# Optimization experiments

Measured on AMD Instinct MI355X. Metric: run time of the kernel, lower is better.

The kernel has to match this reference:

```python
import jax, jax.numpy as jnp
import numpy as np

WINDOW_SIZE, SM, PS = 8, 2, 2  # window_size, spatial_merge_size, patch_size
SMU = SM * SM  # spatial_merge_unit


def _window_index(grid_thw):
    """Numpy port of get_window_index; returns permutation of arange(S)."""
    vmws = WINDOW_SIZE // SM // PS  # 2
    out, wid = [], 0
    for t, h, w in grid_thw:
        lh, lw = h // SM, w // SM
        idx = np.arange(t * lh * lw).reshape(t, lh, lw)
        ph = vmws - lh % vmws
        pw = vmws - lw % vmws
        nh, nw = (lh + ph) // vmws, (lw + pw) // vmws
        pad = np.full((t, lh + ph, lw + pw), -100, dtype=np.int64)
        pad[:, :lh, :lw] = idx
        pad = pad.reshape(t, nh, vmws, nw, vmws).transpose(0, 1, 3, 2, 4).reshape(-1)
        out.append(pad[pad != -100] + wid)
        wid += t * lh * lw
    return np.concatenate(out).astype(np.int32)


def setup_inputs() -> dict:
    key = jax.random.key(0)
    ks = jax.random.split(key, 5)
    B, T, C, H = 1, 16384, 1280, 16
    D = C // H  # 80
    grid_thw = np.array([[1, 256, 256]], dtype=np.int64)  # llm grid 128x128 -> S=16384
    wi = _window_index(grid_thw)
    x = jax.random.normal(ks[0], (B, T, C), jnp.float32)
    cos = jax.random.normal(ks[1], (B * T, 1, D), jnp.float32)
    sin = jax.random.normal(ks[2], (B * T, 1, D), jnp.float32)
    W_qkv = jax.random.normal(ks[3], (C, 3 * C), jnp.float32) * (C ** -0.5)
    W_proj = jax.random.normal(ks[4], (C, C), jnp.float32) * (C ** -0.5)
    # each window: (vmws*vmws) merged tokens * SMU patches = 16 tokens
    block_size = (WINDOW_SIZE // SM // PS) ** 2 * SMU
    return {"x": x, "cos": cos, "sin": sin, "W_qkv": W_qkv, "W_proj": W_proj,
            "window_index": jnp.asarray(wi), "block_size": block_size}


def reference(x, cos, sin, W_qkv, W_proj, window_index, block_size):
    B, T, C = x.shape
    S = B * T
    D = cos.shape[-1]
    H = C // D
    # window reorder (gather)
    xr = x.reshape(S, C)[window_index]
    qkv = (xr @ W_qkv).reshape(S, 3, H, D)
    q, k, v = qkv[:, 0], qkv[:, 1], qkv[:, 2]
    # module's (unusual) q/k mixing 'rotary'
    cw, sw = cos[window_index], sin[window_index]  # (S,1,D) broadcast over heads
    qr = q * cw + k * sw
    kr = k * cw - q * sw
    # block-diagonal attention: uniform 16-token windows -> reshape, no SxS mask
    nb = S // block_size
    qb = qr.reshape(nb, block_size, H, D)
    kb = kr.reshape(nb, block_size, H, D)
    vb = v.reshape(nb, block_size, H, D)
    att = jnp.einsum('bqhd,bkhd->bhqk', qb, kb) * (D ** -0.5)
    att = jax.nn.softmax(att, axis=-1)
    y = jnp.einsum('bhqk,bkhd->bqhd', att, vb).reshape(S, C)
    # undo window reorder
    y = y[jnp.argsort(window_index)]
    return y.reshape(B, T, C) @ W_proj
```

## Files before the change

kernel.cpp:

```cpp
#include <hip/hip_runtime.h>
#include <hip/hip_bf16.h>

#define S_TOK   16384
#define C_DIM   1280
#define C3_DIM  3840
#define H_DIM   16
#define D_DIM   80
#define BLK     16

using u16x8  = __attribute__((ext_vector_type(8))) unsigned short;
using bf16x8 = __attribute__((ext_vector_type(8))) __bf16;
using f32x4  = __attribute__((ext_vector_type(4))) float;

__device__ __forceinline__ unsigned short f2bf(float f) {
    return __bfloat16_as_ushort(__float2bfloat16(f));
}
__device__ __forceinline__ float bf2f(unsigned short u) {
    unsigned int x = (unsigned int)u << 16;
    return __builtin_bit_cast(float, x);
}
__device__ __forceinline__ void gload_lds16(const unsigned short* g, unsigned short* l) {
    __builtin_amdgcn_global_load_lds(
        (const __attribute__((address_space(1))) void*)g,
        (__attribute__((address_space(3))) void*)l, 16, 0, 0);
}

__global__ __launch_bounds__(256) void transpose_cvt(
    const float* __restrict__ W, unsigned short* __restrict__ WT, int K, int N)
{
    __shared__ float tile[32][33];
    const int n0 = blockIdx.x * 32, k0 = blockIdx.y * 32;
    const int tx = threadIdx.x & 31, ty = threadIdx.x >> 5;
#pragma unroll
    for (int i = ty; i < 32; i += 8)
        tile[i][tx] = W[(size_t)(k0 + i) * N + n0 + tx];
    __syncthreads();
#pragma unroll
    for (int i = ty; i < 32; i += 8)
        WT[(size_t)(n0 + i) * K + k0 + tx] = f2bf(tile[tx][i]);
}

__global__ __launch_bounds__(256) void gather_cvt(
    const float* __restrict__ x, const int* __restrict__ wi,
    unsigned short* __restrict__ xg)
{
    int idx = blockIdx.x * 256 + threadIdx.x;
    int s  = idx / 160;
    int c8 = (idx - s * 160) * 8;
    const float* src = x + (size_t)wi[s] * C_DIM + c8;
    f32x4 v0 = *(const f32x4*)src;
    f32x4 v1 = *(const f32x4*)(src + 4);
    u16x8 o;
    o[0]=f2bf(v0[0]); o[1]=f2bf(v0[1]); o[2]=f2bf(v0[2]); o[3]=f2bf(v0[3]);
    o[4]=f2bf(v1[0]); o[5]=f2bf(v1[1]); o[6]=f2bf(v1[2]); o[7]=f2bf(v1[3]);
    *(u16x8*)&xg[(size_t)s * C_DIM + c8] = o;
}

#define TM 128
#define TN 128
#define BK 64

template<bool OUTF32>
__global__ __launch_bounds__(256) void gemm_mfma(
    const unsigned short* __restrict__ A,
    const unsigned short* __restrict__ BT,
    void* __restrict__ Cp,
    int N, int K)
{
    __shared__ __align__(16) unsigned short As[TM * BK];
    __shared__ __align__(16) unsigned short Bs[TN * BK];

    const int m0   = blockIdx.x * TM;
    const int n0   = blockIdx.y * TN;
    const int tid  = threadIdx.x;
    const int lane = tid & 63;
    const int wv   = tid >> 6;
    const int wm   = (wv >> 1) * 64;
    const int wn   = (wv & 1) * 64;
    const int lrow = lane & 15;
    const int quad = lane >> 4;

    int r_[4], csw[4];
#pragma unroll
    for (int c = 0; c < 4; c++) {
        int ch = (wv * 4 + c) * 64 + lane;
        r_[c]  = ch >> 3;
        csw[c] = ((ch & 7) ^ (r_[c] & 7)) << 3;
    }

    int aoff[4], asw[4], boff[4], bsw[4];
#pragma unroll
    for (int t = 0; t < 4; t++) {
        int ra = wm + t * 16 + lrow;
        aoff[t] = ra << 7;  asw[t] = (ra & 7) << 4;
        int rb = wn + t * 16 + lrow;
        boff[t] = rb << 7;  bsw[t] = (rb & 7) << 4;
    }

    f32x4 acc[4][4];
#pragma unroll
    for (int i = 0; i < 4; i++)
#pragma unroll
        for (int j = 0; j < 4; j++)
            acc[i][j] = (f32x4){0.f, 0.f, 0.f, 0.f};

    for (int kt = 0; kt < K; kt += BK) {
#pragma unroll
        for (int c = 0; c < 4; c++)
            gload_lds16(A + (size_t)(m0 + r_[c]) * K + kt + csw[c],
                        As + (wv * 4 + c) * 512);
#pragma unroll
        for (int c = 0; c < 4; c++)
            gload_lds16(BT + (size_t)(n0 + r_[c]) * K + kt + csw[c],
                        Bs + (wv * 4 + c) * 512);
        __syncthreads();

#pragma unroll
        for (int ks = 0; ks < BK; ks += 32) {
            const int cb = (ks << 1) + (quad << 4);
            bf16x8 af[4], bfr[4];
#pragma unroll
            for (int mt = 0; mt < 4; mt++)
                af[mt] = *(const bf16x8*)((const char*)As +
                                          aoff[mt] + (cb ^ asw[mt]));
#pragma unroll
            for (int nt = 0; nt < 4; nt++)
                bfr[nt] = *(const bf16x8*)((const char*)Bs +
                                           boff[nt] + (cb ^ bsw[nt]));
#pragma unroll
            for (int mt = 0; mt < 4; mt++)
#pragma unroll
                for (int nt = 0; nt < 4; nt++)
                    acc[mt][nt] = __builtin_amdgcn_mfma_f32_16x16x32_bf16(
                        af[mt], bfr[nt], acc[mt][nt], 0, 0, 0);
        }
        __syncthreads();
    }

#pragma unroll
    for (int mt = 0; mt < 4; mt++)
#pragma unroll
        for (int nt = 0; nt < 4; nt++)
#pragma unroll
            for (int r = 0; r < 4; r++) {
                int row = m0 + wm + mt * 16 + quad * 4 + r;
                int col = n0 + wn + nt * 16 + lrow;
                if (OUTF32)
                    ((float*)Cp)[(size_t)row * N + col] = acc[mt][nt][r];
                else
                    ((unsigned short*)Cp)[(size_t)row * N + col] =
                        f2bf(acc[mt][nt][r]);
            }
}

__global__ __launch_bounds__(256) void rope_kernel(
    unsigned short* __restrict__ qkv,
    const float* __restrict__ cosp,
    const float* __restrict__ sinp,
    const int* __restrict__ wi)
{
    int idx = blockIdx.x * 256 + threadIdx.x;
    int s  = idx / 160;
    int ch = idx - s * 160;
    int c  = ch * 8;
    int d  = c % D_DIM;
    int src = wi[s];
    const float* cp = cosp + (size_t)src * D_DIM + d;
    const float* sp = sinp + (size_t)src * D_DIM + d;
    f32x4 c0 = *(const f32x4*)cp, c1 = *(const f32x4*)(cp + 4);
    f32x4 s0 = *(const f32x4*)sp, s1 = *(const f32x4*)(sp + 4);
    size_t base = (size_t)s * C3_DIM + c;
    u16x8 qv = *(const u16x8*)(qkv + base);
    u16x8 kv = *(const u16x8*)(qkv + base + C_DIM);
    u16x8 qo, ko;
#pragma unroll
    for (int j = 0; j < 8; j++) {
        float cw = (j < 4) ? c0[j] : c1[j - 4];
        float sw = (j < 4) ? s0[j] : s1[j - 4];
        float q = bf2f(qv[j]), k = bf2f(kv[j]);
        qo[j] = f2bf(q * cw + k * sw);
        ko[j] = f2bf(k * cw - q * sw);
    }
    *(u16x8*)(qkv + base)         = qo;
    *(u16x8*)(qkv + base + C_DIM) = ko;
}

__global__ __launch_bounds__(256) void attn_kernel(
    const unsigned short* __restrict__ qkv,
    unsigned short* __restrict__ y,
    const int* __restrict__ wi)
{
    const int b = blockIdx.x;
    const int h = blockIdx.y;
    __shared__ float qs[BLK][81], ks[BLK][81], vs[BLK][81];
    __shared__ float pr[BLK][17];
    __shared__ int   orow[BLK];
    const int tid = threadIdx.x;

    if (tid < BLK) orow[tid] = wi[b * BLK + tid];
    for (int ch = tid; ch < 480; ch += 256) {
        int which = ch / 160;
        int rem = ch - which * 160;
        int r = rem / 10;
        int c8 = (rem - r * 10) * 8;
        const unsigned short* srcp = qkv +
            (size_t)(b * BLK + r) * C3_DIM + which * C_DIM + h * D_DIM + c8;
        u16x8 v = *(const u16x8*)srcp;
        float* dst = (which == 0) ? &qs[r][c8]
                   : (which == 1) ? &ks[r][c8] : &vs[r][c8];
#pragma unroll
        for (int j = 0; j < 8; j++) dst[j] = bf2f(v[j]);
    }
    __syncthreads();
    {
        int i = tid >> 4, j = tid & 15;
        float a = 0.f;
#pragma unroll
        for (int d = 0; d < D_DIM; d++) a += qs[i][d] * ks[j][d];
        pr[i][j] = a * 0.11180339887498948f;
    }
    __syncthreads();
    if (tid < BLK) {
        float m = -1e30f;
#pragma unroll
        for (int j = 0; j < BLK; j++) m = fmaxf(m, pr[tid][j]);
        float sum = 0.f;
        float e[BLK];
#pragma unroll
        for (int j = 0; j < BLK; j++) { e[j] = __expf(pr[tid][j] - m); sum += e[j]; }
        float inv = 1.f / sum;
#pragma unroll
        for (int j = 0; j < BLK; j++) pr[tid][j] = e[j] * inv;
    }
    __syncthreads();
    for (int i = tid; i < BLK * D_DIM; i += 256) {
        int r = i / D_DIM, d = i - r * D_DIM;
        float a = 0.f;
#pragma unroll
        for (int j = 0; j < BLK; j++) a += pr[r][j] * vs[j][d];
        y[(size_t)orow[r] * C_DIM + h * D_DIM + d] = f2bf(a);
    }
}

extern "C" void kernel_launch(void* const* d_in, const int* in_sizes, int n_in,
                              void* d_out, int out_size, void* d_ws, size_t ws_size,
                              hipStream_t stream)
{
    const float* x     = (const float*)d_in[0];
    const float* cosp  = (const float*)d_in[1];
    const float* sinp  = (const float*)d_in[2];
    const float* Wqkv  = (const float*)d_in[3];
    const float* Wproj = (const float*)d_in[4];
    const int*   wi    = (const int*)d_in[5];

    char* ws = (char*)d_ws;
    unsigned short* qkv    = (unsigned short*)ws;
    unsigned short* yun    = (unsigned short*)(ws + 125829120ull);
    unsigned short* wqkvT  = (unsigned short*)(ws + 167772160ull);
    unsigned short* wprojT = (unsigned short*)(ws + 177602560ull);
    unsigned short* xg     = (unsigned short*)(ws + 180879360ull);

    transpose_cvt<<<dim3(C3_DIM / 32, C_DIM / 32), 256, 0, stream>>>(
        Wqkv, wqkvT, C_DIM, C3_DIM);
    transpose_cvt<<<dim3(C_DIM / 32, C_DIM / 32), 256, 0, stream>>>(
        Wproj, wprojT, C_DIM, C_DIM);

    gather_cvt<<<S_TOK * 160 / 256, 256, 0, stream>>>(x, wi, xg);

    gemm_mfma<false><<<dim3(S_TOK / TM, C3_DIM / TN), 256, 0, stream>>>(
        xg, wqkvT, qkv, C3_DIM, C_DIM);

    rope_kernel<<<S_TOK * 160 / 256, 256, 0, stream>>>(qkv, cosp, sinp, wi);

    attn_kernel<<<dim3(S_TOK / BLK, H_DIM), 256, 0, stream>>>(qkv, yun, wi);

    gemm_mfma<true><<<dim3(S_TOK / TM, C_DIM / TN), 256, 0, stream>>>(
        yun, wprojT, d_out, C_DIM, C_DIM);
}
```

Baseline: 564.4 us.

## Fuse rotary mixing into MFMA-based windowed attention kernel

Drops the separate rope kernel and folds the q/k cos/sin mixing into the attention kernel, so the qkv buffer is no longer rewritten and then read back. Each wavefront now handles one head of one 16-token window. It computes QK^T and P·V with 16x16x32 bf16 MFMA instructions and does the softmax with cross-lane shuffles, removing the LDS staging and barriers. V is read with strided scalar 16-bit loads and the probabilities are rounded to bf16 before the PV product, which costs some precision and may leave the V loads poorly coalesced.

Result: faster. 501.0 us (-11.2%).

```diff
diff --git a/kernel.cpp b/kernel.cpp
--- a/kernel.cpp
+++ b/kernel.cpp
@@ -9,6 +9,7 @@
 #define BLK     16
 
 using u16x8  = __attribute__((ext_vector_type(8))) unsigned short;
+using u16x4  = __attribute__((ext_vector_type(4))) unsigned short;
 using bf16x8 = __attribute__((ext_vector_type(8))) __bf16;
 using f32x4  = __attribute__((ext_vector_type(4))) float;
 
@@ -153,92 +154,108 @@
             }
 }
 
-__global__ __launch_bounds__(256) void rope_kernel(
-    unsigned short* __restrict__ qkv,
+__global__ __launch_bounds__(256) void attn_fused(
+    const unsigned short* __restrict__ qkv,
     const float* __restrict__ cosp,
     const float* __restrict__ sinp,
-    const int* __restrict__ wi)
-{
-    int idx = blockIdx.x * 256 + threadIdx.x;
-    int s  = idx / 160;
-    int ch = idx - s * 160;
-    int c  = ch * 8;
-    int d  = c % D_DIM;
-    int src = wi[s];
-    const float* cp = cosp + (size_t)src * D_DIM + d;
-    const float* sp = sinp + (size_t)src * D_DIM + d;
-    f32x4 c0 = *(const f32x4*)cp, c1 = *(const f32x4*)(cp + 4);
-    f32x4 s0 = *(const f32x4*)sp, s1 = *(const f32x4*)(sp + 4);
-    size_t base = (size_t)s * C3_DIM + c;
-    u16x8 qv = *(const u16x8*)(qkv + base);
-    u16x8 kv = *(const u16x8*)(qkv + base + C_DIM);
-    u16x8 qo, ko;
-#pragma unroll
-    for (int j = 0; j < 8; j++) {
-        float cw = (j < 4) ? c0[j] : c1[j - 4];
-        float sw = (j < 4) ? s0[j] : s1[j - 4];
-        float q = bf2f(qv[j]), k = bf2f(kv[j]);
-        qo[j] = f2bf(q * cw + k * sw);
-        ko[j] = f2bf(k * cw - q * sw);
-    }
-    *(u16x8*)(qkv + base)         = qo;
-    *(u16x8*)(qkv + base + C_DIM) = ko;
-}
-
-__global__ __launch_bounds__(256) void attn_kernel(
-    const unsigned short* __restrict__ qkv,
-    unsigned short* __restrict__ y,
-    const int* __restrict__ wi)
-{
-    const int b = blockIdx.x;
-    const int h = blockIdx.y;
-    __shared__ float qs[BLK][81], ks[BLK][81], vs[BLK][81];
-    __shared__ float pr[BLK][17];
-    __shared__ int   orow[BLK];
-    const int tid = threadIdx.x;
-
-    if (tid < BLK) orow[tid] = wi[b * BLK + tid];
-    for (int ch = tid; ch < 480; ch += 256) {
-        int which = ch / 160;
-        int rem = ch - which * 160;
-        int r = rem / 10;
-        int c8 = (rem - r * 10) * 8;
-        const unsigned short* srcp = qkv +
-            (size_t)(b * BLK + r) * C3_DIM + which * C_DIM + h * D_DIM + c8;
-        u16x8 v = *(const u16x8*)srcp;
-        float* dst = (which == 0) ? &qs[r][c8]
-                   : (which == 1) ? &ks[r][c8] : &vs[r][c8];
-#pragma unroll
-        for (int j = 0; j < 8; j++) dst[j] = bf2f(v[j]);
-    }
-    __syncthreads();
-    {
-        int i = tid >> 4, j = tid & 15;
-        float a = 0.f;
-#pragma unroll
-        for (int d = 0; d < D_DIM; d++) a += qs[i][d] * ks[j][d];
-        pr[i][j] = a * 0.11180339887498948f;
-    }
-    __syncthreads();
-    if (tid < BLK) {
-        float m = -1e30f;
-#pragma unroll
-        for (int j = 0; j < BLK; j++) m = fmaxf(m, pr[tid][j]);
-        float sum = 0.f;
-        float e[BLK];
-#pragma unroll
-        for (int j = 0; j < BLK; j++) { e[j] = __expf(pr[tid][j] - m); sum += e[j]; }
-        float inv = 1.f / sum;
-#pragma unroll
-        for (int j = 0; j < BLK; j++) pr[tid][j] = e[j] * inv;
-    }
-    __syncthreads();
-    for (int i = tid; i < BLK * D_DIM; i += 256) {
-        int r = i / D_DIM, d = i - r * D_DIM;
-        float a = 0.f;
-#pragma unroll
-        for (int j = 0; j < BLK; j++) a += pr[r][j] * vs[j][d];
-        y[(size_t)orow[r] * C_DIM + h * D_DIM + d] = f2bf(a);
+    const int* __restrict__ wi,
+    unsigned short* __restrict__ y)
+{
+    const int wave = threadIdx.x >> 6;
+    const int lane = threadIdx.x & 63;
+    const int b    = blockIdx.y;
+    const int h    = blockIdx.x * 4 + wave;
+    const int j16  = lane & 15;
+    const int quad = lane >> 4;
+
+    const int    srow = b * BLK + j16;
+    const int    crow = wi[srow];
+    const size_t qoff = (size_t)srow * C3_DIM + h * D_DIM;
+
+    const unsigned short* vbase =
+        qkv + (size_t)b * BLK * C3_DIM + 2 * C_DIM + h * D_DIM + j16;
+    u16x8 vraw[5];
+#pragma unroll
+    for (int t = 0; t < 5; t++) {
+#pragma unroll
+        for (int e = 0; e < 8; e++) {
+            int kks = (quad < 2) ? (quad * 8 + e) : e;
+            unsigned short rv = vbase[(size_t)kks * C3_DIM + t * 16];
+            vraw[t][e] = (quad < 2) ? rv : (unsigned short)0;
+        }
+    }
+
+    const unsigned short* qrow = qkv + qoff;
+    const float* cr = cosp + (size_t)crow * D_DIM;
+    const float* sr = sinp + (size_t)crow * D_DIM;
+    bf16x8 qf[3], kf[3];
+#pragma unroll
+    for (int s = 0; s < 3; s++) {
+        int d = 32 * s + quad * 8;
+        bool valid = (d < D_DIM);
+        int dc = valid ? d : 0;
+        u16x8 qv = *(const u16x8*)(qrow + dc);
+        u16x8 kv = *(const u16x8*)(qrow + C_DIM + dc);
+        f32x4 c0 = *(const f32x4*)(cr + dc);
+        f32x4 c1 = *(const f32x4*)(cr + dc + 4);
+        f32x4 s0 = *(const f32x4*)(sr + dc);
+        f32x4 s1 = *(const f32x4*)(sr + dc + 4);
+        u16x8 qo, ko;
+#pragma unroll
+        for (int j = 0; j < 8; j++) {
+            float cw = (j < 4) ? c0[j] : c1[j - 4];
+            float sw = (j < 4) ? s0[j] : s1[j - 4];
+            float q = bf2f(qv[j]), k = bf2f(kv[j]);
+            qo[j] = valid ? f2bf(q * cw + k * sw) : (unsigned short)0;
+            ko[j] = valid ? f2bf(k * cw - q * sw) : (unsigned short)0;
+        }
+        qf[s] = __builtin_bit_cast(bf16x8, qo);
+        kf[s] = __builtin_bit_cast(bf16x8, ko);
+    }
+
+    f32x4 sacc = (f32x4){0.f, 0.f, 0.f, 0.f};
+#pragma unroll
+    for (int s = 0; s < 3; s++)
+        sacc = __builtin_amdgcn_mfma_f32_16x16x32_bf16(kf[s], qf[s], sacc, 0, 0, 0);
+
+    const float scale = 0.11180339887498948f;
+    float sc[4];
+#pragma unroll
+    for (int r = 0; r < 4; r++) sc[r] = sacc[r] * scale;
+    float m = fmaxf(fmaxf(sc[0], sc[1]), fmaxf(sc[2], sc[3]));
+    m = fmaxf(m, __shfl_xor(m, 16));
+    m = fmaxf(m, __shfl_xor(m, 32));
+    float e[4], sum = 0.f;
+#pragma unroll
+    for (int r = 0; r < 4; r++) { e[r] = __expf(sc[r] - m); sum += e[r]; }
+    sum += __shfl_xor(sum, 16);
+    sum += __shfl_xor(sum, 32);
+    float inv = 1.f / sum;
+
+    int sl = quad * 32 + j16;
+    float pv0[4], pv1[4];
+#pragma unroll
+    for (int r = 0; r < 4; r++) pv0[r] = __shfl(e[r], sl & 63);
+#pragma unroll
+    for (int r = 0; r < 4; r++) pv1[r] = __shfl(e[r], (sl + 16) & 63);
+    u16x8 pf;
+#pragma unroll
+    for (int r = 0; r < 4; r++) {
+        pf[r]     = (quad < 2) ? f2bf(pv0[r]) : (unsigned short)0;
+        pf[r + 4] = (quad < 2) ? f2bf(pv1[r]) : (unsigned short)0;
+    }
+    bf16x8 pfrag = __builtin_bit_cast(bf16x8, pf);
+
+    unsigned short* yrow = y + (size_t)crow * C_DIM + h * D_DIM + quad * 4;
+#pragma unroll
+    for (int t = 0; t < 5; t++) {
+        f32x4 o = __builtin_amdgcn_mfma_f32_16x16x32_bf16(
+            __builtin_bit_cast(bf16x8, vraw[t]), pfrag,
+            (f32x4){0.f, 0.f, 0.f, 0.f}, 0, 0, 0);
+        u16x4 ov;
+#pragma unroll
+        for (int r = 0; r < 4; r++) ov[r] = f2bf(o[r] * inv);
+        *(u16x4*)(yrow + t * 16) = ov;
     }
 }
 
@@ -270,9 +287,8 @@
     gemm_mfma<false><<<dim3(S_TOK / TM, C3_DIM / TN), 256, 0, stream>>>(
         xg, wqkvT, qkv, C3_DIM, C_DIM);
 
-    rope_kernel<<<S_TOK * 160 / 256, 256, 0, stream>>>(qkv, cosp, sinp, wi);
-
-    attn_kernel<<<dim3(S_TOK / BLK, H_DIM), 256, 0, stream>>>(qkv, yun, wi);
+    attn_fused<<<dim3(H_DIM / 4, S_TOK / BLK), 256, 0, stream>>>(
+        qkv, cosp, sinp, wi, yun);
 
     gemm_mfma<true><<<dim3(S_TOK / TM, C_DIM / TN), 256, 0, stream>>>(
         yun, wprojT, d_out, C_DIM, C_DIM);
```
